# Kernel optimization log

Hardware: AMD Instinct MI355X
Metric: run time of the kernel (lower is better)

## Reference

```python
import jax, jax.numpy as jnp
import numpy as np
from jax import lax

B, H, W, C = 8, 64, 64, 64
NW, K, NH = 4, 3, 4
WS = 32            # window size = 64 / sqrt(4)
L = H * W
K2 = K * K
DH = C // NH
D = C * K2         # 576


def adaptive_avg_pool2d(x, oh, ow):
    # torch AdaptiveAvgPool2d semantics: bin i = [floor(i*L/o), ceil((i+1)*L/o))
    Hi, Wi = x.shape[-2], x.shape[-1]
    rows = [x[..., (i * Hi) // oh: -(-((i + 1) * Hi) // oh), :].mean(-2) for i in range(oh)]
    x = jnp.stack(rows, axis=-2)
    cols = [x[..., (j * Wi) // ow: -(-((j + 1) * Wi) // ow)].mean(-1) for j in range(ow)]
    return jnp.stack(cols, axis=-1)


def _forward(x, attn, proj_v_w, proj_v_b, proj_out_w, proj_out_b,
             down_w, down_b, lin1_w, lin1_b, lin2_w, lin2_b,
             gk_w, gk_b, fusion_w, fusion_b):
    x4 = x.reshape(B, H, W, C)
    # window partition -> (B*NW, C, WS, WS)
    xw = x4.reshape(B, H // WS, WS, W // WS, WS, C).transpose(0, 1, 3, 2, 4, 5)
    xw = xw.reshape(B * NW, WS, WS, C).transpose(0, 3, 1, 2)
    # pooled per-window kernels -> (B, NW, C*K*K)
    kern = adaptive_avg_pool2d(xw, K, K).reshape(B, NW, D)
    kv = kern @ proj_v_w.T + proj_v_b
    kv = kv.reshape(B, NW, NH, DH, K2).transpose(0, 1, 2, 4, 3).reshape(B * NW * NH, K2, DH)
    # pooled attention; the AdaptiveAvgPool1d(nW) on length-nW axis is identity
    aqk = adaptive_avg_pool2d(attn, K2, K2).reshape(B * NW * NH, K2, K2)
    kern = jnp.matmul(aqk, kv)  # (B*NW*NH, K2, DH)
    # faithful to original: flattened (B,NW,NH) reinterpreted as (B,NH,NW)
    kern = kern.reshape(B, NH, NW, K2, DH).transpose(0, 2, 1, 4, 3).reshape(B, NW, D)
    kern = (kern @ proj_out_w.T + proj_out_b).reshape(B, NW, C, K, K)
    # window-kernel reweighting (squeeze-excite over windows)
    pooled = xw.reshape(B, NW, C, WS, WS).mean(axis=(3, 4))          # (B, NW, C)
    ww = jnp.einsum('bnc,nc->bn', pooled, down_w) + down_b           # grouped 1x1 conv
    ww = jax.nn.gelu(ww @ lin1_w.T + lin1_b, approximate=False)
    weight = jax.nn.sigmoid(ww @ lin2_w.T + lin2_b)                  # (B, NW)
    kern = kern * weight[:, :, None, None, None]
    # global kernel: 1x1 conv over the window axis
    gk = jnp.einsum('bnckl,n->bckl', kern, gk_w) + gk_b              # (B, C, K, K)
    all_k = jnp.concatenate([kern, gk[:, None]], axis=1)             # (B, NW+1, C, K, K)
    all_k = all_k.reshape(B * (NW + 1) * C, 1, K, K)
    # depthwise conv with per-(batch,window,channel) dynamic kernels
    xc = x4.transpose(0, 3, 1, 2)                                    # (B, C, H, W)
    xr = jnp.tile(xc, (1, NW + 1, 1, 1)).reshape(1, B * (NW + 1) * C, H, W)
    out = lax.conv_general_dilated(xr, all_k, (1, 1), ((1, 1), (1, 1)),
                                   feature_group_count=B * (NW + 1) * C,
                                   dimension_numbers=('NCHW', 'OIHW', 'NCHW'))
    out = out.reshape(B, (NW + 1) * C, H, W)
    out = jnp.einsum('bihw,oi->bohw', out, fusion_w) + fusion_b[None, :, None, None]
    return out.transpose(0, 2, 3, 1).reshape(B, L, C)


def setup_inputs() -> dict:
    key = jax.random.key(0)
    ks = jax.random.split(key, 10)
    s = 0.02
    f32 = jnp.float32
    return {
        'x': jax.random.normal(ks[0], (B, L, C), f32),
        'attn': jax.random.normal(ks[1], (B * NW, NH, WS * WS, WS * WS), f32),
        'proj_v_w': jax.random.normal(ks[2], (D, D), f32) * s,
        'proj_v_b': jnp.zeros((D,), f32),
        'proj_out_w': jax.random.normal(ks[3], (D, D), f32) * s,
        'proj_out_b': jnp.zeros((D,), f32),
        'down_w': jax.random.normal(ks[4], (NW, C), f32) * s,
        'down_b': jnp.zeros((NW,), f32),
        'lin1_w': jax.random.normal(ks[5], (4 * NW, NW), f32) * s,
        'lin1_b': jnp.zeros((4 * NW,), f32),
        'lin2_w': jax.random.normal(ks[6], (NW, 4 * NW), f32) * s,
        'lin2_b': jnp.zeros((NW,), f32),
        'gk_w': jax.random.normal(ks[7], (NW,), f32) * s,
        'gk_b': jnp.zeros((), f32),
        'fusion_w': jax.random.normal(ks[8], (C, (NW + 1) * C), f32) * s,
        'fusion_b': jnp.zeros((C,), f32),
    }


def reference(x, attn, proj_v_w, proj_v_b, proj_out_w, proj_out_b,
              down_w, down_b, lin1_w, lin1_b, lin2_w, lin2_b,
              gk_w, gk_b, fusion_w, fusion_b):
    return _forward(x, attn, proj_v_w, proj_v_b, proj_out_w, proj_out_b,
                    down_w, down_b, lin1_w, lin1_b, lin2_w, lin2_b,
                    gk_w, gk_b, fusion_w, fusion_b)
```

## Files before the change

kernel.cpp:

```cpp
#include <hip/hip_runtime.h>
#include <cstdint>

#define NB 8
#define NL 4096
#define NC 64
#define NWIN 4
#define NHEAD 4
#define DD 576

#define OFF_AQK   0
#define OFF_KV    10368
#define OFF_K2O   28800
#define ZERO_FLOATS 47232
#define OFF_KERN0 47232
#define OFF_KERNM 65664
#define OFF_WW    84096
#define OFF_WT    84128
#define OFF_F2    84160

__global__ __launch_bounds__(256) void k_attn_pool(const float* __restrict__ attn,
                                                   float* __restrict__ aqk_sum) {
    __shared__ float acc[81];
    int t = threadIdx.x;
    if (t < 81) acc[t] = 0.f;
    __syncthreads();

    int mat = blockIdx.x >> 4;
    int chunk = blockIdx.x & 15;
    int wave = t >> 6, lane = t & 63;
    const float* base = attn + (size_t)mat * 1024u * 1024u;
    int c0 = lane * 16;
    int b0 = (c0 * 9) >> 10;

    for (int rr = 0; rr < 16; ++rr) {
        int r = chunk * 64 + wave * 16 + rr;
        const float4* row = reinterpret_cast<const float4*>(base + (size_t)r * 1024 + c0);
        float a0 = 0.f, a1 = 0.f;
#pragma unroll
        for (int u = 0; u < 4; ++u) {
            float4 v = row[u];
            float vals[4] = {v.x, v.y, v.z, v.w};
#pragma unroll
            for (int e = 0; e < 4; ++e) {
                int c = c0 + u * 4 + e;
                float val = vals[e];
                int p = (c * 9) >> 10;
                if (p == b0) a0 += val; else a1 += val;
                int ns = ((p + 1) << 10) / 9;
                if (c == ns) a1 += val;
            }
        }
        int rp = (r * 9) >> 10;
        int rs = ((rp + 1) << 10) / 9;
        atomicAdd(&acc[rp * 9 + b0], a0);
        if (a1 != 0.f && b0 < 8) atomicAdd(&acc[rp * 9 + b0 + 1], a1);
        if (r == rs && rp < 8) {
            atomicAdd(&acc[(rp + 1) * 9 + b0], a0);
            if (a1 != 0.f && b0 < 8) atomicAdd(&acc[(rp + 1) * 9 + b0 + 1], a1);
        }
    }
    __syncthreads();
    if (t < 81) {
        float v = acc[t];
        if (v != 0.f) atomicAdd(&aqk_sum[mat * 81 + t], v);
    }
}

__global__ __launch_bounds__(640) void k_win_pool(const float* __restrict__ x,
                                                  const float* __restrict__ down_w,
                                                  const float* __restrict__ down_b,
                                                  float* __restrict__ kern0,
                                                  float* __restrict__ ww) {
    int blk = blockIdx.x;
    int b = blk >> 2, nw = blk & 3;
    int wr = nw >> 1, wc = nw & 1;
    int wave = threadIdx.x >> 6, c = threadIdx.x & 63;
    const float* xb = x + (size_t)b * NL * NC;

    if (wave < 9) {
        int ki = wave / 3, kj = wave % 3;
        int si = (ki * 32) / 3, ei = ((ki + 1) * 32 + 2) / 3;
        int sj = (kj * 32) / 3, ej = ((kj + 1) * 32 + 2) / 3;
        float s = 0.f;
        for (int i = si; i < ei; ++i)
            for (int j = sj; j < ej; ++j)
                s += xb[((size_t)((wr * 32 + i) * 64) + wc * 32 + j) * 64 + c];
        float cnt = (float)((ei - si) * (ej - sj));
        kern0[blk * DD + c * 9 + wave] = s / cnt;
    } else {
        float s = 0.f;
        for (int i = 0; i < 32; ++i)
            for (int j = 0; j < 32; ++j)
                s += xb[((size_t)((wr * 32 + i) * 64) + wc * 32 + j) * 64 + c];
        float v = (s * (1.f / 1024.f)) * down_w[nw * 64 + c];
#pragma unroll
        for (int off = 32; off; off >>= 1) v += __shfl_down(v, off);
        if (c == 0) ww[blk] = v + down_b[nw];
    }
}

__global__ void k_mlp(const float* __restrict__ ww,
                      const float* __restrict__ lin1_w, const float* __restrict__ lin1_b,
                      const float* __restrict__ lin2_w, const float* __restrict__ lin2_b,
                      float* __restrict__ weight) {
    int b = threadIdx.x;
    if (b >= NB) return;
    float w0[4];
#pragma unroll
    for (int n = 0; n < 4; ++n) w0[n] = ww[b * 4 + n];
    float acc2[4];
#pragma unroll
    for (int n = 0; n < 4; ++n) acc2[n] = lin2_b[n];
    for (int j = 0; j < 16; ++j) {
        float h = lin1_b[j];
#pragma unroll
        for (int n = 0; n < 4; ++n) h += w0[n] * lin1_w[j * 4 + n];
        h = 0.5f * h * (1.f + erff(h * 0.70710678118654752440f));
#pragma unroll
        for (int n = 0; n < 4; ++n) acc2[n] += h * lin2_w[n * 16 + j];
    }
#pragma unroll
    for (int n = 0; n < 4; ++n) weight[b * 4 + n] = 1.f / (1.f + expf(-acc2[n]));
}

__global__ __launch_bounds__(256) void k_mm576(const float* __restrict__ A,
                                               const float* __restrict__ Wm,
                                               const float* __restrict__ bias,
                                               float* __restrict__ out) {
    __shared__ float Ws[64][65];
    __shared__ float As[32][65];
    int oc = blockIdx.x % 9, ic = blockIdx.x / 9;
    int o0 = oc * 64, i0 = ic * 64;
    int t = threadIdx.x;
    for (int idx = t; idx < 64 * 64; idx += 256) {
        int j = idx >> 6, ii = idx & 63;
        Ws[j][ii] = Wm[(size_t)(o0 + j) * DD + i0 + ii];
    }
    for (int idx = t; idx < 32 * 64; idx += 256) {
        int r = idx >> 6, ii = idx & 63;
        As[r][ii] = A[r * DD + i0 + ii];
    }
    __syncthreads();
    int j = t & 63, rg = t >> 6;
    float acc[8];
#pragma unroll
    for (int q = 0; q < 8; ++q) acc[q] = 0.f;
    for (int ii = 0; ii < 64; ++ii) {
        float w = Ws[j][ii];
#pragma unroll
        for (int q = 0; q < 8; ++q) acc[q] += As[rg * 8 + q][ii] * w;
    }
    float bo = (ic == 0) ? bias[o0 + j] : 0.f;
#pragma unroll
    for (int q = 0; q < 8; ++q)
        atomicAdd(&out[(rg * 8 + q) * DD + o0 + j], acc[q] + bo);
}

__global__ __launch_bounds__(576) void k_pmm(const float* __restrict__ aqk_sum,
                                             const float* __restrict__ kv,
                                             float* __restrict__ kernM) {
    int blk = blockIdx.x;
    int b = blk >> 2, n = blk & 3;
    int d = threadIdx.x;
    int i = d / 144, rem = d % 144, dh = rem / 9, k2 = rem % 9;
    int f = b * 16 + i * 4 + n;
    int sk = (k2 * 1024) / 9, ek = ((k2 + 1) * 1024 + 8) / 9;
    float rlk = (float)(ek - sk);
    const float* aq = aqk_sum + f * 81 + k2 * 9;
    const float* kvp = kv + (b * 4 + i) * DD + n * 144 + dh * 9;
    float acc = 0.f;
#pragma unroll
    for (int q = 0; q < 9; ++q) {
        int sq = (q * 1024) / 9, eq = ((q + 1) * 1024 + 8) / 9;
        float inv = 1.f / (rlk * (float)(eq - sq));
        acc += aq[q] * inv * kvp[q];
    }
    kernM[blk * DD + d] = acc;
}

__global__ __launch_bounds__(576) void k_build_F(const float* __restrict__ kern2,
                                                 const float* __restrict__ weight,
                                                 const float* __restrict__ gk_w,
                                                 const float* __restrict__ gk_b,
                                                 const float* __restrict__ fusion_w,
                                                 float* __restrict__ F2) {
    int b = blockIdx.x;
    int d = threadIdx.x;
    int c = d / 9, kl = d % 9;
    float k2s[4];
    float g = gk_b[0];
#pragma unroll
    for (int n = 0; n < 4; ++n) {
        float v = kern2[(b * 4 + n) * DD + d] * weight[b * 4 + n];
        k2s[n] = v;
        g += v * gk_w[n];
    }
    size_t obase = (((size_t)b * 64 + c) * 9 + kl) * 64;
    for (int o = 0; o < 64; ++o) {
        float v = fusion_w[o * 320 + 256 + c] * g;
#pragma unroll
        for (int n = 0; n < 4; ++n) v += fusion_w[o * 320 + n * 64 + c] * k2s[n];
        F2[obase + o] = v;
    }
}

__global__ __launch_bounds__(256) void k_conv(const float* __restrict__ x,
                                              const float* __restrict__ F2,
                                              const float* __restrict__ fusion_b,
                                              float* __restrict__ out) {
    __shared__ float As[3][16][68];
    __shared__ float Bs[16][9][64];
    int t = threadIdx.x;
    int h = blockIdx.x & 63, b = blockIdx.x >> 6;
    int w0 = (t & 15) * 4;
    int o0 = (t >> 4) * 4;

    float acc[4][4];
#pragma unroll
    for (int wi = 0; wi < 4; ++wi)
#pragma unroll
        for (int oi = 0; oi < 4; ++oi) acc[wi][oi] = 0.f;

    for (int cq = 0; cq < 4; ++cq) {
        __syncthreads();
        for (int idx = t; idx < 16 * 9 * 64; idx += 256) {
            int o = idx & 63; int r = idx >> 6; int kl = r % 9; int cc = r / 9;
            Bs[cc][kl][o] = F2[(((size_t)b * 64 + cq * 16 + cc) * 9 + kl) * 64 + o];
        }
        for (int idx = t; idx < 3 * 64 * 4; idx += 256) {
            int gg = idx & 3; int w = (idx >> 2) & 63; int dk = idx >> 8;
            int hh = h + dk - 1;
            float4 v = make_float4(0.f, 0.f, 0.f, 0.f);
            if (hh >= 0 && hh < 64)
                v = *reinterpret_cast<const float4*>(
                    &x[(((size_t)b * 64 + hh) * 64 + w) * 64 + cq * 16 + gg * 4]);
            As[dk][gg * 4 + 0][w + 1] = v.x;
            As[dk][gg * 4 + 1][w + 1] = v.y;
            As[dk][gg * 4 + 2][w + 1] = v.z;
            As[dk][gg * 4 + 3][w + 1] = v.w;
        }
        if (t < 96) {
            int cc = t & 15; int dk = (t >> 4) % 3; int side = t / 48;
            As[dk][cc][side ? 65 : 0] = 0.f;
        }
        __syncthreads();

#pragma unroll
        for (int dk = 0; dk < 3; ++dk) {
#pragma unroll 4
            for (int cc = 0; cc < 16; ++cc) {
                float4 xa = *reinterpret_cast<const float4*>(&As[dk][cc][w0]);
                float xv[6];
                xv[0] = xa.x; xv[1] = xa.y; xv[2] = xa.z; xv[3] = xa.w;
                xv[4] = As[dk][cc][w0 + 4];
                xv[5] = As[dk][cc][w0 + 5];
#pragma unroll
                for (int dl = 0; dl < 3; ++dl) {
                    float4 bv = *reinterpret_cast<const float4*>(&Bs[cc][dk * 3 + dl][o0]);
#pragma unroll
                    for (int wi = 0; wi < 4; ++wi) {
                        float xx = xv[wi + dl];
                        acc[wi][0] += xx * bv.x;
                        acc[wi][1] += xx * bv.y;
                        acc[wi][2] += xx * bv.z;
                        acc[wi][3] += xx * bv.w;
                    }
                }
            }
        }
    }

    float4 fb = *reinterpret_cast<const float4*>(&fusion_b[o0]);
#pragma unroll
    for (int wi = 0; wi < 4; ++wi) {
        float4 r;
        r.x = acc[wi][0] + fb.x;
        r.y = acc[wi][1] + fb.y;
        r.z = acc[wi][2] + fb.z;
        r.w = acc[wi][3] + fb.w;
        *reinterpret_cast<float4*>(
            &out[(((size_t)b * NL) + h * 64 + w0 + wi) * 64 + o0]) = r;
    }
}

extern "C" void kernel_launch(void* const* d_in, const int* in_sizes, int n_in,
                              void* d_out, int out_size, void* d_ws, size_t ws_size,
                              hipStream_t stream) {
    const float* x         = (const float*)d_in[0];
    const float* attn      = (const float*)d_in[1];
    const float* proj_v_w  = (const float*)d_in[2];
    const float* proj_v_b  = (const float*)d_in[3];
    const float* proj_out_w= (const float*)d_in[4];
    const float* proj_out_b= (const float*)d_in[5];
    const float* down_w    = (const float*)d_in[6];
    const float* down_b    = (const float*)d_in[7];
    const float* lin1_w    = (const float*)d_in[8];
    const float* lin1_b    = (const float*)d_in[9];
    const float* lin2_w    = (const float*)d_in[10];
    const float* lin2_b    = (const float*)d_in[11];
    const float* gk_w      = (const float*)d_in[12];
    const float* gk_b      = (const float*)d_in[13];
    const float* fusion_w  = (const float*)d_in[14];
    const float* fusion_b  = (const float*)d_in[15];
    float* out = (float*)d_out;
    float* ws  = (float*)d_ws;
    (void)in_sizes; (void)n_in; (void)out_size; (void)ws_size;

    float* aqk   = ws + OFF_AQK;
    float* kv    = ws + OFF_KV;
    float* kern2 = ws + OFF_K2O;
    float* kern0 = ws + OFF_KERN0;
    float* kernM = ws + OFF_KERNM;
    float* wwb   = ws + OFF_WW;
    float* wt    = ws + OFF_WT;
    float* F2    = ws + OFF_F2;

    hipMemsetAsync(ws, 0, ZERO_FLOATS * sizeof(float), stream);

    k_attn_pool<<<2048, 256, 0, stream>>>(attn, aqk);
    k_win_pool<<<32, 640, 0, stream>>>(x, down_w, down_b, kern0, wwb);
    k_mlp<<<1, 64, 0, stream>>>(wwb, lin1_w, lin1_b, lin2_w, lin2_b, wt);
    k_mm576<<<81, 256, 0, stream>>>(kern0, proj_v_w, proj_v_b, kv);
    k_pmm<<<32, 576, 0, stream>>>(aqk, kv, kernM);
    k_mm576<<<81, 256, 0, stream>>>(kernM, proj_out_w, proj_out_b, kern2);
    k_build_F<<<8, 576, 0, stream>>>(kern2, wt, gk_w, gk_b, fusion_w, F2);
    k_conv<<<512, 256, 0, stream>>>(x, F2, fusion_b, out);
}
```

Before: 849.9 us.

## Coalesce attn pooling loads, parallelize window pooling, fold MLP into build_F

The attention pooling kernel now loads each row with per-wave contiguous float4 accesses. It replaces per-element branches with precomputed column and row masks and keeps register accumulators, so atomics happen once per thread instead of once per row. Window pooling uses 1024 threads that each read float4 channel groups across rows, reducing into shared memory with atomics. The MLP kernel is merged into k_build_F, which also stages fusion_w transposed in shared memory and writes F2 with coalesced o-contiguous stores. Shared-memory atomics and a large LDS footprint in build_F are added in exchange.

```diff
diff --git a/kernel.cpp b/kernel.cpp
--- a/kernel.cpp
+++ b/kernel.cpp
@@ -15,112 +15,166 @@
 #define OFF_KERN0 47232
 #define OFF_KERNM 65664
 #define OFF_WW    84096
-#define OFF_WT    84128
 #define OFF_F2    84160
 
 __global__ __launch_bounds__(256) void k_attn_pool(const float* __restrict__ attn,
                                                    float* __restrict__ aqk_sum) {
-    __shared__ float acc[81];
+    __shared__ float accL[81];
     int t = threadIdx.x;
-    if (t < 81) acc[t] = 0.f;
+    if (t < 81) accL[t] = 0.f;
     __syncthreads();
 
     int mat = blockIdx.x >> 4;
     int chunk = blockIdx.x & 15;
     int wave = t >> 6, lane = t & 63;
-    const float* base = attn + (size_t)mat * 1024u * 1024u;
-    int c0 = lane * 16;
-    int b0 = (c0 * 9) >> 10;
+    const float* base = attn + (size_t)mat * 1048576u;
+
+    float cm0[4][4], cm1[4][4];
+    int b0s[4];
+#pragma unroll
+    for (int s = 0; s < 4; ++s) {
+        int c0 = s * 256 + lane * 4;
+        int b0 = (c0 * 9) >> 10;
+        b0s[s] = b0;
+#pragma unroll
+        for (int e = 0; e < 4; ++e) {
+            int c = c0 + e;
+            int p = (c * 9) >> 10;
+            int ns = ((p + 1) << 10) / 9;
+            bool sh = (c == ns);
+            cm0[s][e] = (p == b0) ? 1.f : 0.f;
+            cm1[s][e] = ((p == b0 + 1) || (p == b0 && sh)) ? 1.f : 0.f;
+        }
+    }
+
+    int r0 = chunk * 64 + wave * 16;
+    int rb0 = (r0 * 9) >> 10;
+    float a00[4] = {0.f, 0.f, 0.f, 0.f};
+    float a01[4] = {0.f, 0.f, 0.f, 0.f};
+    float a10[4] = {0.f, 0.f, 0.f, 0.f};
+    float a11[4] = {0.f, 0.f, 0.f, 0.f};
 
     for (int rr = 0; rr < 16; ++rr) {
-        int r = chunk * 64 + wave * 16 + rr;
-        const float4* row = reinterpret_cast<const float4*>(base + (size_t)r * 1024 + c0);
-        float a0 = 0.f, a1 = 0.f;
-#pragma unroll
-        for (int u = 0; u < 4; ++u) {
-            float4 v = row[u];
-            float vals[4] = {v.x, v.y, v.z, v.w};
-#pragma unroll
-            for (int e = 0; e < 4; ++e) {
-                int c = c0 + u * 4 + e;
-                float val = vals[e];
-                int p = (c * 9) >> 10;
-                if (p == b0) a0 += val; else a1 += val;
-                int ns = ((p + 1) << 10) / 9;
-                if (c == ns) a1 += val;
-            }
-        }
+        int r = r0 + rr;
+        const float4* rowp = reinterpret_cast<const float4*>(base + (size_t)r * 1024);
+        float4 vv[4];
+        vv[0] = rowp[lane];
+        vv[1] = rowp[64 + lane];
+        vv[2] = rowp[128 + lane];
+        vv[3] = rowp[192 + lane];
         int rp = (r * 9) >> 10;
         int rs = ((rp + 1) << 10) / 9;
-        atomicAdd(&acc[rp * 9 + b0], a0);
-        if (a1 != 0.f && b0 < 8) atomicAdd(&acc[rp * 9 + b0 + 1], a1);
-        if (r == rs && rp < 8) {
-            atomicAdd(&acc[(rp + 1) * 9 + b0], a0);
-            if (a1 != 0.f && b0 < 8) atomicAdd(&acc[(rp + 1) * 9 + b0 + 1], a1);
-        }
-    }
-    __syncthreads();
-    if (t < 81) {
-        float v = acc[t];
-        if (v != 0.f) atomicAdd(&aqk_sum[mat * 81 + t], v);
-    }
-}
-
-__global__ __launch_bounds__(640) void k_win_pool(const float* __restrict__ x,
-                                                  const float* __restrict__ down_w,
-                                                  const float* __restrict__ down_b,
-                                                  float* __restrict__ kern0,
-                                                  float* __restrict__ ww) {
+        float mf0 = (rp == rb0) ? 1.f : 0.f;
+        float mf1 = ((rp == rb0 + 1) || (rp == rb0 && r == rs)) ? 1.f : 0.f;
+#pragma unroll
+        for (int s = 0; s < 4; ++s) {
+            float cl0 = vv[s].x * cm0[s][0] + vv[s].y * cm0[s][1]
+                      + vv[s].z * cm0[s][2] + vv[s].w * cm0[s][3];
+            float cl1 = vv[s].x * cm1[s][0] + vv[s].y * cm1[s][1]
+                      + vv[s].z * cm1[s][2] + vv[s].w * cm1[s][3];
+            a00[s] += cl0 * mf0;
+            a01[s] += cl1 * mf0;
+            a10[s] += cl0 * mf1;
+            a11[s] += cl1 * mf1;
+        }
+    }
+
+#pragma unroll
+    for (int s = 0; s < 4; ++s) {
+        int cb = b0s[s];
+        atomicAdd(&accL[rb0 * 9 + cb], a00[s]);
+        if (cb < 8 && a01[s] != 0.f) atomicAdd(&accL[rb0 * 9 + cb + 1], a01[s]);
+        if (rb0 < 8) {
+            if (a10[s] != 0.f) atomicAdd(&accL[(rb0 + 1) * 9 + cb], a10[s]);
+            if (cb < 8 && a11[s] != 0.f) atomicAdd(&accL[(rb0 + 1) * 9 + cb + 1], a11[s]);
+        }
+    }
+    __syncthreads();
+    if (t < 81) atomicAdd(&aqk_sum[mat * 81 + t], accL[t]);
+}
+
+__global__ __launch_bounds__(1024) void k_win_pool(const float* __restrict__ x,
+                                                   const float* __restrict__ down_w,
+                                                   const float* __restrict__ down_b,
+                                                   float* __restrict__ kern0,
+                                                   float* __restrict__ ww) {
+    __shared__ float sums[3][3][64];
+    __shared__ float tot[64];
+    int t = threadIdx.x;
+    if (t < 576) ((float*)sums)[t] = 0.f;
+    else if (t < 640) tot[t - 576] = 0.f;
+    __syncthreads();
+
     int blk = blockIdx.x;
     int b = blk >> 2, nw = blk & 3;
     int wr = nw >> 1, wc = nw & 1;
-    int wave = threadIdx.x >> 6, c = threadIdx.x & 63;
-    const float* xb = x + (size_t)b * NL * NC;
-
-    if (wave < 9) {
-        int ki = wave / 3, kj = wave % 3;
-        int si = (ki * 32) / 3, ei = ((ki + 1) * 32 + 2) / 3;
-        int sj = (kj * 32) / 3, ej = ((kj + 1) * 32 + 2) / 3;
-        float s = 0.f;
-        for (int i = si; i < ei; ++i)
-            for (int j = sj; j < ej; ++j)
-                s += xb[((size_t)((wr * 32 + i) * 64) + wc * 32 + j) * 64 + c];
-        float cnt = (float)((ei - si) * (ej - sj));
-        kern0[blk * DD + c * 9 + wave] = s / cnt;
-    } else {
-        float s = 0.f;
-        for (int i = 0; i < 32; ++i)
-            for (int j = 0; j < 32; ++j)
-                s += xb[((size_t)((wr * 32 + i) * 64) + wc * 32 + j) * 64 + c];
-        float v = (s * (1.f / 1024.f)) * down_w[nw * 64 + c];
+    int c4 = t & 15, j = (t >> 4) & 31, s = t >> 9;
+    const float* xb = x + ((size_t)b * NL + (size_t)(wr * 32) * 64 + wc * 32 + j) * 64 + c4 * 4;
+
+    int q = (3 * j) >> 5;
+    int js = ((q + 1) << 5) / 3;
+    bool csh = (j == js);
+    float cw[3];
+#pragma unroll
+    for (int k = 0; k < 3; ++k)
+        cw[k] = ((k == q) || (csh && k == q + 1)) ? 1.f : 0.f;
+
+    float acc[3][3][4];
+#pragma unroll
+    for (int rb = 0; rb < 3; ++rb)
+#pragma unroll
+        for (int cb = 0; cb < 3; ++cb)
+#pragma unroll
+            for (int ch = 0; ch < 4; ++ch) acc[rb][cb][ch] = 0.f;
+    float ts[4] = {0.f, 0.f, 0.f, 0.f};
+
+    for (int i = 0; i < 16; ++i) {
+        int r = s * 16 + i;
+        float4 v = *reinterpret_cast<const float4*>(xb + (size_t)r * 4096);
+        ts[0] += v.x; ts[1] += v.y; ts[2] += v.z; ts[3] += v.w;
+        int rp = (3 * r) >> 5;
+        int rsb = ((rp + 1) << 5) / 3;
+        bool rsh = (r == rsb);
+#pragma unroll
+        for (int rb = 0; rb < 3; ++rb) {
+            if (rb == rp || (rsh && rb == rp + 1)) {
+#pragma unroll
+                for (int cb = 0; cb < 3; ++cb) {
+                    acc[rb][cb][0] += v.x * cw[cb];
+                    acc[rb][cb][1] += v.y * cw[cb];
+                    acc[rb][cb][2] += v.z * cw[cb];
+                    acc[rb][cb][3] += v.w * cw[cb];
+                }
+            }
+        }
+    }
+
+#pragma unroll
+    for (int rb = 0; rb < 3; ++rb)
+#pragma unroll
+        for (int cb = 0; cb < 3; ++cb)
+#pragma unroll
+            for (int ch = 0; ch < 4; ++ch) {
+                float v = acc[rb][cb][ch];
+                if (v != 0.f) atomicAdd(&sums[rb][cb][c4 * 4 + ch], v);
+            }
+#pragma unroll
+    for (int ch = 0; ch < 4; ++ch) atomicAdd(&tot[c4 * 4 + ch], ts[ch]);
+    __syncthreads();
+
+    if (t < 576) {
+        int c = t / 9, rem = t % 9, ki = rem / 3, kj = rem % 3;
+        const float cnt0 = 11.f, cnt1 = 12.f;
+        float rc = (ki == 1) ? cnt1 : cnt0;
+        float cc = (kj == 1) ? cnt1 : cnt0;
+        kern0[(size_t)blk * DD + t] = sums[ki][kj][c] / (rc * cc);
+    }
+    if (t < 64) {
+        float v = tot[t] * (1.f / 1024.f) * down_w[nw * 64 + t];
 #pragma unroll
         for (int off = 32; off; off >>= 1) v += __shfl_down(v, off);
-        if (c == 0) ww[blk] = v + down_b[nw];
-    }
-}
-
-__global__ void k_mlp(const float* __restrict__ ww,
-                      const float* __restrict__ lin1_w, const float* __restrict__ lin1_b,
-                      const float* __restrict__ lin2_w, const float* __restrict__ lin2_b,
-                      float* __restrict__ weight) {
-    int b = threadIdx.x;
-    if (b >= NB) return;
-    float w0[4];
-#pragma unroll
-    for (int n = 0; n < 4; ++n) w0[n] = ww[b * 4 + n];
-    float acc2[4];
-#pragma unroll
-    for (int n = 0; n < 4; ++n) acc2[n] = lin2_b[n];
-    for (int j = 0; j < 16; ++j) {
-        float h = lin1_b[j];
-#pragma unroll
-        for (int n = 0; n < 4; ++n) h += w0[n] * lin1_w[j * 4 + n];
-        h = 0.5f * h * (1.f + erff(h * 0.70710678118654752440f));
-#pragma unroll
-        for (int n = 0; n < 4; ++n) acc2[n] += h * lin2_w[n * 16 + j];
-    }
-#pragma unroll
-    for (int n = 0; n < 4; ++n) weight[b * 4 + n] = 1.f / (1.f + expf(-acc2[n]));
+        if (t == 0) ww[blk] = v + down_b[nw];
+    }
 }
 
 __global__ __launch_bounds__(256) void k_mm576(const float* __restrict__ A,
@@ -179,28 +233,64 @@
 }
 
 __global__ __launch_bounds__(576) void k_build_F(const float* __restrict__ kern2,
-                                                 const float* __restrict__ weight,
+                                                 const float* __restrict__ wwb,
+                                                 const float* __restrict__ lin1_w,
+                                                 const float* __restrict__ lin1_b,
+                                                 const float* __restrict__ lin2_w,
+                                                 const float* __restrict__ lin2_b,
                                                  const float* __restrict__ gk_w,
                                                  const float* __restrict__ gk_b,
                                                  const float* __restrict__ fusion_w,
                                                  float* __restrict__ F2) {
+    __shared__ float fwT[320][65];
+    __shared__ float k2L[4 * DD];
+    __shared__ float hL[16];
+    __shared__ float wt[4];
     int b = blockIdx.x;
-    int d = threadIdx.x;
-    int c = d / 9, kl = d % 9;
-    float k2s[4];
-    float g = gk_b[0];
-#pragma unroll
-    for (int n = 0; n < 4; ++n) {
-        float v = kern2[(b * 4 + n) * DD + d] * weight[b * 4 + n];
-        k2s[n] = v;
-        g += v * gk_w[n];
-    }
-    size_t obase = (((size_t)b * 64 + c) * 9 + kl) * 64;
-    for (int o = 0; o < 64; ++o) {
-        float v = fusion_w[o * 320 + 256 + c] * g;
-#pragma unroll
-        for (int n = 0; n < 4; ++n) v += fusion_w[o * 320 + n * 64 + c] * k2s[n];
-        F2[obase + o] = v;
+    int t = threadIdx.x;
+
+    const float4* fw4 = reinterpret_cast<const float4*>(fusion_w);
+    for (int idx = t; idx < 5120; idx += 576) {
+        int o = idx / 80, i4 = idx % 80;
+        float4 v = fw4[idx];
+        fwT[i4 * 4 + 0][o] = v.x;
+        fwT[i4 * 4 + 1][o] = v.y;
+        fwT[i4 * 4 + 2][o] = v.z;
+        fwT[i4 * 4 + 3][o] = v.w;
+    }
+    for (int idx = t; idx < 4 * DD; idx += 576)
+        k2L[idx] = kern2[(size_t)b * 4 * DD + idx];
+    if (t < 16) {
+        float h = lin1_b[t];
+#pragma unroll
+        for (int n = 0; n < 4; ++n) h += wwb[b * 4 + n] * lin1_w[t * 4 + n];
+        hL[t] = 0.5f * h * (1.f + erff(h * 0.70710678118654752440f));
+    }
+    __syncthreads();
+    if (t < 4) {
+        float a = lin2_b[t];
+        for (int jj = 0; jj < 16; ++jj) a += hL[jj] * lin2_w[t * 16 + jj];
+        wt[t] = 1.f / (1.f + expf(-a));
+    }
+    __syncthreads();
+
+    int o = t & 63, dg = t >> 6;
+    float gw0 = gk_w[0], gw1 = gk_w[1], gw2 = gk_w[2], gw3 = gk_w[3];
+    float gkb = gk_b[0];
+    float w0 = wt[0], w1 = wt[1], w2 = wt[2], w3 = wt[3];
+    int c = (dg * 64) / 9, kl = (dg * 64) % 9;
+    for (int dd = 0; dd < 64; ++dd) {
+        int d = dg * 64 + dd;
+        float s0 = k2L[d] * w0;
+        float s1 = k2L[DD + d] * w1;
+        float s2 = k2L[2 * DD + d] * w2;
+        float s3 = k2L[3 * DD + d] * w3;
+        float g = gkb + s0 * gw0 + s1 * gw1 + s2 * gw2 + s3 * gw3;
+        float val = fwT[c][o] * s0 + fwT[64 + c][o] * s1
+                  + fwT[128 + c][o] * s2 + fwT[192 + c][o] * s3
+                  + fwT[256 + c][o] * g;
+        F2[((size_t)b * DD + d) * 64 + o] = val;
+        if (++kl == 9) { kl = 0; ++c; }
     }
 }
 
@@ -312,17 +402,16 @@
     float* kern0 = ws + OFF_KERN0;
     float* kernM = ws + OFF_KERNM;
     float* wwb   = ws + OFF_WW;
-    float* wt    = ws + OFF_WT;
     float* F2    = ws + OFF_F2;
 
     hipMemsetAsync(ws, 0, ZERO_FLOATS * sizeof(float), stream);
 
     k_attn_pool<<<2048, 256, 0, stream>>>(attn, aqk);
-    k_win_pool<<<32, 640, 0, stream>>>(x, down_w, down_b, kern0, wwb);
-    k_mlp<<<1, 64, 0, stream>>>(wwb, lin1_w, lin1_b, lin2_w, lin2_b, wt);
+    k_win_pool<<<32, 1024, 0, stream>>>(x, down_w, down_b, kern0, wwb);
     k_mm576<<<81, 256, 0, stream>>>(kern0, proj_v_w, proj_v_b, kv);
     k_pmm<<<32, 576, 0, stream>>>(aqk, kv, kernM);
     k_mm576<<<81, 256, 0, stream>>>(kernM, proj_out_w, proj_out_b, kern2);
-    k_build_F<<<8, 576, 0, stream>>>(kern2, wt, gk_w, gk_b, fusion_w, F2);
+    k_build_F<<<8, 576, 0, stream>>>(kern2, wwb, lin1_w, lin1_b, lin2_w, lin2_b,
+                                     gk_w, gk_b, fusion_w, F2);
     k_conv<<<512, 256, 0, stream>>>(x, F2, fusion_b, out);
 }
```

Measured after the change: 824.0 us. 1.03x faster.
